# Optimization experiments

Hardware: AMD Instinct MI355X
Metric: run time of the kernel (lower is better)

Reference implementation:

```python
import jax, jax.numpy as jnp
import numpy as np

B, M, E, K = 8, 256, 128, 16
H, A, R, RMS = 1024, 256, 1024, 512
NEG = -1e25


def setup_inputs() -> dict:
    key = jax.random.key(0)
    ks = jax.random.split(key, 12)
    inp = {
        "mention_reprs": jax.random.normal(ks[0], (B, M, H), jnp.float32),
        "entities": jax.random.randint(ks[1], (B, E, K), 0, M),
        "entity_masks": jax.random.randint(ks[2], (B, E, K), 0, 2, dtype=jnp.int32),
        "relation_memory": jax.random.normal(ks[3], (R, RMS), jnp.float32),
        # GatedMILAttention params
        "Wv": jax.random.normal(ks[4], (A, H), jnp.float32) / np.sqrt(H),
        "bv": jnp.zeros((A,), jnp.float32),
        "Wu": jax.random.normal(ks[5], (A, H), jnp.float32) / np.sqrt(H),
        "bu": jnp.zeros((A,), jnp.float32),
        "Wa": jax.random.normal(ks[6], (1, A), jnp.float32) / np.sqrt(A),
        "ba": jnp.zeros((1,), jnp.float32),
        # relation memory read linear: Linear(RMS, H)
        "Wr": jax.random.normal(ks[7], (H, RMS), jnp.float32) / np.sqrt(RMS),
        "br": jnp.zeros((H,), jnp.float32),
        # output linear: Linear(H + RMS, H)
        "Wo": jax.random.normal(ks[8], (H, H + RMS), jnp.float32) / np.sqrt(H + RMS),
        "bo": jnp.zeros((H,), jnp.float32),
    }
    return inp


def reference(mention_reprs, entities, entity_masks, relation_memory,
              Wv, bv, Wu, bu, Wa, ba, Wr, br, Wo, bo):
    # gather mention clusters: [B, E, K, H]
    clusters = jax.vmap(lambda m, e: m[e])(mention_reprs, entities)
    # gated MIL attention
    aV = jnp.tanh(jnp.einsum('bekh,ah->beka', clusters, Wv) + bv)
    aU = jax.nn.sigmoid(jnp.einsum('bekh,ah->beka', clusters, Wu) + bu)
    logits = jnp.einsum('beka,oa->beko', aV * aU, Wa) + ba  # [B,E,K,1]
    mask = entity_masks[..., None].astype(bool)
    logits = jnp.where(mask, logits, NEG)
    a = jax.nn.softmax(logits, axis=2)
    # weighted pooling over mentions: [B, E, H]
    entity_reprs = jnp.sum(a * clusters, axis=2)
    # relation memory read (memory detached for the read projection)
    s_w = jax.lax.stop_gradient(relation_memory) @ Wr.T + br        # [R, H]
    s = jnp.einsum('beh,rh->ber', entity_reprs, s_w)                # [B, E, R]
    s = jnp.einsum('ber,rm->bem', s, relation_memory)               # [B, E, RMS]
    out = jnp.concatenate([entity_reprs, s], axis=-1) @ Wo.T + bo   # [B, E, H]
    return out  # dropout is identity at inference
```

## Files before the change

### kernel.cpp

```cpp
#include <hip/hip_runtime.h>
#include <cstdint>
#include <cstddef>

#define NEG_ (-1e25f)

typedef __bf16 bf16x8 __attribute__((ext_vector_type(8)));
typedef float  f32x4  __attribute__((ext_vector_type(4)));
typedef short  s16x8  __attribute__((ext_vector_type(8)));
typedef const __attribute__((address_space(1))) void* gas_t;
typedef __attribute__((address_space(3))) void* las_t;

#define MFMA16 __builtin_amdgcn_mfma_f32_16x16x32_bf16

__device__ __forceinline__ short f2bf(float f) {
  union { float f; unsigned u; } v; v.f = f;
  unsigned r = v.u + 0x7fffu + ((v.u >> 16) & 1u);
  return (short)(r >> 16);
}

__device__ __forceinline__ float bf2f(short s) {
  union { unsigned u; float f; } t; t.u = ((unsigned)(unsigned short)s) << 16;
  return t.f;
}

__device__ __forceinline__ s16x8 cvt8(const float* s) {
  bf16x8 r;
  #pragma unroll
  for (int j = 0; j < 8; ++j) r[j] = (__bf16)s[j];
  union { bf16x8 b; s16x8 s; } u; u.b = r; return u.s;
}

__device__ __forceinline__ void gload(const short* g, short* l) {
  __builtin_amdgcn_global_load_lds((gas_t)g, (las_t)l, 16, 0, 0);
}

struct Params {
  const float* ment; const int* ents; const int* msk;
  const float* rm; const float* Wv; const float* bv; const float* Wu;
  const float* bu; const float* Wa; const float* Wr; const float* br;
  const float* Wo; const float* bo; float* out;
  short *Xb, *Wvb, *Wub, *rmb, *Wrb, *Wo2b, *Wo1b, *swTb, *Ub, *Weffb, *erb;
  float *wpart, *cf, *gw2;
};

__global__ __launch_bounds__(256) void k0(Params p) {
  const int g = blockIdx.x * 256 + threadIdx.x;
  #pragma unroll
  for (int it = 0; it < 4; ++it) {
    int u = g + it * 131072;
    long e = (long)u * 8;
    const float* src; short* dst;
    if (u < 262144)      { src = p.ment + e;                     dst = p.Xb + e; }
    else if (u < 294912) { long o = e - 2097152; src = p.Wv + o; dst = p.Wvb + o; }
    else if (u < 327680) { long o = e - 2359296; src = p.Wu + o; dst = p.Wub + o; }
    else if (u < 393216) { long o = e - 2621440; src = p.rm + o; dst = p.rmb + o; }
    else if (u < 458752) { long o = e - 3145728; src = p.Wr + o; dst = p.Wrb + o; }
    else                 { long o = e - 3670016;
                           src = p.Wo + (o >> 9) * 1536 + 1024 + (o & 511);
                           dst = p.Wo2b + o; }
    float t[8];
    *(float4*)t       = *(const float4*)src;
    *(float4*)(t + 4) = *(const float4*)(src + 4);
    *(s16x8*)dst = cvt8(t);
  }
}

template <int NT, int EPI>
__device__ void g64(const short* __restrict__ A, int lda,
                    const short* __restrict__ B, int ldb,
                    void* __restrict__ C, int ldc, int m0, int n0,
                    const short* __restrict__ w1, const float* __restrict__ e0,
                    const float* __restrict__ e1, const float* __restrict__ e2,
                    short* lds) {
  short* As = lds;
  short* Bs = lds + 16384;
  const int tid = threadIdx.x, wave = tid >> 6, lane = tid & 63;
  const int quad = lane >> 4, l16 = lane & 15;
  const int wm = (wave & 1) * 32, wn = (wave >> 1) * 32;
  const int srow = tid >> 2, scol = (tid & 3) * 8;
  const short* Ag = A + (long)(m0 + srow) * lda + scol;
  const short* Bg = B + (long)(n0 + srow) * ldb + scol;
  const int wb = wave * 512;
  auto issue = [&](int kt) {
    int buf = kt & 7; int ko = kt * 32;
    gload(Ag + ko, As + buf * 2048 + wb);
    gload(Bg + ko, Bs + buf * 2048 + wb);
  };
  f32x4 acc[2][2] = {};
  issue(0); issue(1); issue(2); issue(3); issue(4); issue(5);
  for (int kt = 0; kt < NT; ++kt) {
    int rem = NT - 1 - kt;
    if (rem >= 5)      asm volatile("s_waitcnt vmcnt(10)" ::: "memory");
    else if (rem == 4) asm volatile("s_waitcnt vmcnt(8)" ::: "memory");
    else if (rem == 3) asm volatile("s_waitcnt vmcnt(6)" ::: "memory");
    else if (rem == 2) asm volatile("s_waitcnt vmcnt(4)" ::: "memory");
    else if (rem == 1) asm volatile("s_waitcnt vmcnt(2)" ::: "memory");
    else               asm volatile("s_waitcnt vmcnt(0)" ::: "memory");
    asm volatile("s_barrier" ::: "memory");
    if (kt + 6 < NT) issue(kt + 6);
    const short* as = As + (kt & 7) * 2048;
    const short* bs = Bs + (kt & 7) * 2048;
    bf16x8 a0 = *(const bf16x8*)&as[(wm + l16) * 32 + quad * 8];
    bf16x8 a1 = *(const bf16x8*)&as[(wm + 16 + l16) * 32 + quad * 8];
    bf16x8 b0 = *(const bf16x8*)&bs[(wn + l16) * 32 + quad * 8];
    bf16x8 b1 = *(const bf16x8*)&bs[(wn + 16 + l16) * 32 + quad * 8];
    acc[0][0] = MFMA16(a0, b0, acc[0][0], 0, 0, 0);
    acc[0][1] = MFMA16(a0, b1, acc[0][1], 0, 0, 0);
    acc[1][0] = MFMA16(a1, b0, acc[1][0], 0, 0, 0);
    acc[1][1] = MFMA16(a1, b1, acc[1][1], 0, 0, 0);
  }
  #pragma unroll
  for (int i = 0; i < 2; ++i)
    #pragma unroll
    for (int j = 0; j < 2; ++j) {
      int col = n0 + wn + j * 16 + l16;
      #pragma unroll
      for (int r = 0; r < 4; ++r) {
        int row = m0 + wm + i * 16 + quad * 4 + r;
        float v = acc[i][j][r];
        if constexpr (EPI == 0) {
          ((short*)C)[(long)row * ldc + col] = f2bf(v);
        } else if constexpr (EPI == 1) {
          v += bf2f(w1[(long)row * 1024 + col]);
          ((short*)C)[(long)row * ldc + col] = f2bf(v);
        } else {
          v += e0[col] + e1[row] * e2[col];
          ((float*)C)[(long)row * ldc + col] = v;
        }
      }
    }
}

__device__ void vu_ring(int mi, int ni, const Params& p, short* lds, float* red) {
  short* As  = lds;
  short* Bvs = lds + 6 * 1024;
  short* Bus = lds + 6 * 1024 + 6 * 2048;
  const int tid = threadIdx.x, wave = tid >> 6, lane = tid & 63;
  const int quad = lane >> 4, l16 = lane & 15;
  const int wm = (wave & 1) * 16, wn = (wave >> 1) * 32;
  const int m0 = mi * 32, n0 = ni * 64;
  const int srow = tid >> 2, scol = (tid & 3) * 8;
  const short* Ag  = p.Xb  + (long)(m0 + srow) * 1024 + scol;
  const short* Bvg = p.Wvb + (long)(n0 + srow) * 1024 + scol;
  const short* Bug = p.Wub + (long)(n0 + srow) * 1024 + scol;
  const int wb = wave * 512;
  auto issue = [&](int kt) {
    int buf = kt % 6; int ko = kt * 32;
    if (wave < 2)
      gload(Ag + ko, As + buf * 1024 + wb);
    gload(Bvg + ko, Bvs + buf * 2048 + wb);
    gload(Bug + ko, Bus + buf * 2048 + wb);
  };
  f32x4 accv[2] = {}, accu[2] = {};
  issue(0); issue(1); issue(2); issue(3);
  for (int kt = 0; kt < 32; ++kt) {
    int rem = 31 - kt;
    if (wave < 2) {
      if (rem >= 3)      asm volatile("s_waitcnt vmcnt(9)" ::: "memory");
      else if (rem == 2) asm volatile("s_waitcnt vmcnt(6)" ::: "memory");
      else if (rem == 1) asm volatile("s_waitcnt vmcnt(3)" ::: "memory");
      else               asm volatile("s_waitcnt vmcnt(0)" ::: "memory");
    } else {
      if (rem >= 3)      asm volatile("s_waitcnt vmcnt(6)" ::: "memory");
      else if (rem == 2) asm volatile("s_waitcnt vmcnt(4)" ::: "memory");
      else if (rem == 1) asm volatile("s_waitcnt vmcnt(2)" ::: "memory");
      else               asm volatile("s_waitcnt vmcnt(0)" ::: "memory");
    }
    asm volatile("s_barrier" ::: "memory");
    if (kt + 4 < 32) issue(kt + 4);
    const short* as  = As  + (kt % 6) * 1024;
    const short* bvs = Bvs + (kt % 6) * 2048;
    const short* bus = Bus + (kt % 6) * 2048;
    bf16x8 af = *(const bf16x8*)&as[(wm + l16) * 32 + quad * 8];
    bf16x8 v0 = *(const bf16x8*)&bvs[(wn + l16) * 32 + quad * 8];
    bf16x8 v1 = *(const bf16x8*)&bvs[(wn + 16 + l16) * 32 + quad * 8];
    bf16x8 u0 = *(const bf16x8*)&bus[(wn + l16) * 32 + quad * 8];
    bf16x8 u1 = *(const bf16x8*)&bus[(wn + 16 + l16) * 32 + quad * 8];
    accv[0] = MFMA16(af, v0, accv[0], 0, 0, 0);
    accv[1] = MFMA16(af, v1, accv[1], 0, 0, 0);
    accu[0] = MFMA16(af, u0, accu[0], 0, 0, 0);
    accu[1] = MFMA16(af, u1, accu[1], 0, 0, 0);
  }
  float wsum[4] = {0.f, 0.f, 0.f, 0.f};
  #pragma unroll
  for (int j = 0; j < 2; ++j) {
    int col = n0 + wn + j * 16 + l16;
    float bvc = p.bv[col], buc = p.bu[col], wac = p.Wa[col];
    #pragma unroll
    for (int r = 0; r < 4; ++r) {
      float vv = tanhf(accv[j][r] + bvc);
      float uu = accu[j][r] + buc;
      wsum[r] += (vv / (1.0f + expf(-uu))) * wac;
    }
  }
  #pragma unroll
  for (int r = 0; r < 4; ++r) {
    float s = wsum[r];
    s += __shfl_down(s, 8, 16);
    s += __shfl_down(s, 4, 16);
    s += __shfl_down(s, 2, 16);
    s += __shfl_down(s, 1, 16);
    if (l16 == 0) red[(wave >> 1) * 32 + wm + quad * 4 + r] = s;
  }
  __syncthreads();
  if (tid < 32) p.wpart[ni * 2048 + m0 + tid] = red[tid] + red[32 + tid];
}

__device__ void gw2_wave(int row, const Params& p) {
  const int lane = threadIdx.x & 63;
  const short* u = p.Ub + (long)row * 1024 + lane * 16;
  union { s16x8 s; bf16x8 b; } w0, w1;
  w0.s = *(const s16x8*)u;
  w1.s = *(const s16x8*)(u + 8);
  float s = 0.f;
  #pragma unroll
  for (int j = 0; j < 8; ++j) s += (float)w0.b[j] + (float)w1.b[j];
  #pragma unroll
  for (int off = 32; off > 0; off >>= 1) s += __shfl_down(s, off);
  if (lane == 0) p.gw2[row] = s;
}

__device__ void entity_wave(int be, const Params& p) {
  const int lane = threadIdx.x & 63;
  const int b = be >> 7;
  float a = NEG_; int idx = 0;
  if (lane < 16) {
    idx = p.ents[be * 16 + lane];
    int j = (b << 8) + idx;
    float lw = p.wpart[j] + p.wpart[2048 + j] + p.wpart[4096 + j] + p.wpart[6144 + j];
    a = p.msk[be * 16 + lane] ? lw : NEG_;
  }
  float m = a;
  m = fmaxf(m, __shfl_xor(m, 1, 16));
  m = fmaxf(m, __shfl_xor(m, 2, 16));
  m = fmaxf(m, __shfl_xor(m, 4, 16));
  m = fmaxf(m, __shfl_xor(m, 8, 16));
  float e = expf(a - m);
  float s = e;
  s += __shfl_xor(s, 1, 16);
  s += __shfl_xor(s, 2, 16);
  s += __shfl_xor(s, 4, 16);
  s += __shfl_xor(s, 8, 16);
  float aw = e / s;
  float ak[16]; int ik[16];
  #pragma unroll
  for (int k = 0; k < 16; ++k) { ak[k] = __shfl(aw, k); ik[k] = __shfl(idx, k); }
  const short* Xr = p.Xb + ((long)b << 18);
  const int h0 = lane * 16;
  float acc[16];
  #pragma unroll
  for (int t = 0; t < 16; ++t) acc[t] = 0.f;
  #pragma unroll
  for (int c = 0; c < 2; ++c) {
    s16x8 xv[8][2];
    #pragma unroll
    for (int k = 0; k < 8; ++k) {
      const short* xr = Xr + (long)ik[c * 8 + k] * 1024 + h0;
      xv[k][0] = *(const s16x8*)xr;
      xv[k][1] = *(const s16x8*)(xr + 8);
    }
    #pragma unroll
    for (int k = 0; k < 8; ++k) {
      union { s16x8 s; bf16x8 b; } u0, u1;
      u0.s = xv[k][0]; u1.s = xv[k][1];
      float akk = ak[c * 8 + k];
      #pragma unroll
      for (int t = 0; t < 8; ++t) {
        acc[t]     += akk * (float)u0.b[t];
        acc[8 + t] += akk * (float)u1.b[t];
      }
    }
  }
  short* er = p.erb + (long)be * 1024 + h0;
  *(s16x8*)er       = cvt8(acc);
  *(s16x8*)(er + 8) = cvt8(acc + 8);
  float c = 0.f;
  const float* brp = p.br + h0;
  #pragma unroll
  for (int t = 0; t < 16; ++t) c += acc[t] * brp[t];
  #pragma unroll
  for (int off = 32; off > 0; off >>= 1) c += __shfl_down(c, off);
  if (lane == 0) p.cf[be] = c;
}

__global__ __launch_bounds__(256) void k1(Params p) {
  __shared__ short lds[32768];
  __shared__ float red[64];
  const int blk = blockIdx.x;
  if (blk < 256) {
    vu_ring(blk & 63, blk >> 6, p, lds, red);
  } else if (blk < 512) {
    int q = blk - 256;
    g64<16, 0>(p.Wrb, 512, p.rmb, 512, p.swTb, 1024,
               (q >> 4) * 64, (q & 15) * 64, nullptr, nullptr, nullptr, nullptr, lds);
  } else if (blk < 768) {
    int q = blk - 512;
    g64<16, 0>(p.Wo2b, 512, p.rmb, 512, p.Ub, 1024,
               (q >> 4) * 64, (q & 15) * 64, nullptr, nullptr, nullptr, nullptr, lds);
  } else {
    int g = (blk - 768) * 256 + threadIdx.x;
    #pragma unroll
    for (int it = 0; it < 8; ++it) {
      long o = ((long)(g + it * 16384)) * 8;
      const float* src = p.Wo + (o >> 10) * 1536 + (o & 1023);
      float t[8];
      *(float4*)t       = *(const float4*)src;
      *(float4*)(t + 4) = *(const float4*)(src + 4);
      *(s16x8*)(p.Wo1b + o) = cvt8(t);
    }
  }
}

__global__ __launch_bounds__(256) void k2(Params p) {
  __shared__ short lds[32768];
  const int blk = blockIdx.x;
  if (blk < 256) {
    g64<32, 1>(p.Ub, 1024, p.swTb, 1024, p.Weffb, 1024,
               (blk >> 4) * 64, (blk & 15) * 64, p.Wo1b, nullptr, nullptr, nullptr, lds);
  } else {
    int q = blk - 256;
    int wave = threadIdx.x >> 6;
    gw2_wave(q * 4 + wave, p);
    entity_wave(q * 4 + wave, p);
  }
}

__global__ __launch_bounds__(256) void k3(Params p) {
  __shared__ short lds[32768];
  const int blk = blockIdx.x;
  g64<32, 2>(p.erb, 1024, p.Weffb, 1024, p.out, 1024,
             (blk >> 4) * 64, (blk & 15) * 64, nullptr, p.bo, p.cf, p.gw2, lds);
}

extern "C" void kernel_launch(void* const* d_in, const int* in_sizes, int n_in,
                              void* d_out, int out_size, void* d_ws, size_t ws_size,
                              hipStream_t stream) {
  (void)in_sizes; (void)n_in; (void)out_size; (void)ws_size;
  Params p;
  p.ment = (const float*)d_in[0];
  p.ents = (const int*)d_in[1];
  p.msk  = (const int*)d_in[2];
  p.rm   = (const float*)d_in[3];
  p.Wv   = (const float*)d_in[4];
  p.bv   = (const float*)d_in[5];
  p.Wu   = (const float*)d_in[6];
  p.bu   = (const float*)d_in[7];
  p.Wa   = (const float*)d_in[8];
  p.Wr   = (const float*)d_in[10];
  p.br   = (const float*)d_in[11];
  p.Wo   = (const float*)d_in[12];
  p.bo   = (const float*)d_in[13];
  p.out  = (float*)d_out;

  char* w = (char*)d_ws;
  auto alloc = [&](size_t bytes) {
    void* q = (void*)w; w += (bytes + 255) & ~(size_t)255; return q;
  };
  p.Xb    = (short*)alloc((size_t)2048 * 1024 * 2);
  p.Wvb   = (short*)alloc((size_t)256 * 1024 * 2);
  p.Wub   = (short*)alloc((size_t)256 * 1024 * 2);
  p.rmb   = (short*)alloc((size_t)1024 * 512 * 2);
  p.Wrb   = (short*)alloc((size_t)1024 * 512 * 2);
  p.Wo2b  = (short*)alloc((size_t)1024 * 512 * 2);
  p.Wo1b  = (short*)alloc((size_t)1024 * 1024 * 2);
  p.swTb  = (short*)alloc((size_t)1024 * 1024 * 2);
  p.Ub    = (short*)alloc((size_t)1024 * 1024 * 2);
  p.Weffb = (short*)alloc((size_t)1024 * 1024 * 2);
  p.erb   = (short*)alloc((size_t)1024 * 1024 * 2);
  p.wpart = (float*)alloc((size_t)4 * 2048 * 4);
  p.cf    = (float*)alloc((size_t)1024 * 4);
  p.gw2   = (float*)alloc((size_t)1024 * 4);

  k0<<<512, 256, 0, stream>>>(p);
  k1<<<832, 256, 0, stream>>>(p);
  k2<<<512, 256, 0, stream>>>(p);
  k3<<<256, 256, 0, stream>>>(p);
}
```

Baseline: 130.8 us.

## Use 64x32 tiles for K2/K3 GEMMs, read Wo fp32 in epilogue, shrink LDS rings

Adds a 64x32-tile GEMM variant for the Weff and output GEMMs, doubling their block counts to 512 so more CUs are filled. The Weff epilogue now adds the fp32 Wo left half directly instead of a bf16 copy, so k1 no longer converts Wo1 and the Wo1b buffer is gone. Pipeline rings are cut from 8 to 6 stages (g64) and from 6 to 5 (vu_ring), with shallower prefetch, which lowers LDS per block and should allow more resident blocks. The trade-off is less latency hiding per block, lower MFMA reuse per tile, and uncoalesced strided fp32 reads of Wo in the epilogue.

```diff
diff --git a/kernel.cpp b/kernel.cpp
--- a/kernel.cpp
+++ b/kernel.cpp
@@ -18,11 +18,6 @@
   return (short)(r >> 16);
 }
 
-__device__ __forceinline__ float bf2f(short s) {
-  union { unsigned u; float f; } t; t.u = ((unsigned)(unsigned short)s) << 16;
-  return t.f;
-}
-
 __device__ __forceinline__ s16x8 cvt8(const float* s) {
   bf16x8 r;
   #pragma unroll
@@ -39,7 +34,7 @@
   const float* rm; const float* Wv; const float* bv; const float* Wu;
   const float* bu; const float* Wa; const float* Wr; const float* br;
   const float* Wo; const float* bo; float* out;
-  short *Xb, *Wvb, *Wub, *rmb, *Wrb, *Wo2b, *Wo1b, *swTb, *Ub, *Weffb, *erb;
+  short *Xb, *Wvb, *Wub, *rmb, *Wrb, *Wo2b, *swTb, *Ub, *Weffb, *erb;
   float *wpart, *cf, *gw2;
 };
 
@@ -65,15 +60,12 @@
   }
 }
 
-template <int NT, int EPI>
 __device__ void g64(const short* __restrict__ A, int lda,
                     const short* __restrict__ B, int ldb,
-                    void* __restrict__ C, int ldc, int m0, int n0,
-                    const short* __restrict__ w1, const float* __restrict__ e0,
-                    const float* __restrict__ e1, const float* __restrict__ e2,
+                    short* __restrict__ C, int ldc, int NT, int m0, int n0,
                     short* lds) {
   short* As = lds;
-  short* Bs = lds + 16384;
+  short* Bs = lds + 12288;
   const int tid = threadIdx.x, wave = tid >> 6, lane = tid & 63;
   const int quad = lane >> 4, l16 = lane & 15;
   const int wm = (wave & 1) * 32, wn = (wave >> 1) * 32;
@@ -82,24 +74,22 @@
   const short* Bg = B + (long)(n0 + srow) * ldb + scol;
   const int wb = wave * 512;
   auto issue = [&](int kt) {
-    int buf = kt & 7; int ko = kt * 32;
+    int buf = kt % 6; int ko = kt * 32;
     gload(Ag + ko, As + buf * 2048 + wb);
     gload(Bg + ko, Bs + buf * 2048 + wb);
   };
   f32x4 acc[2][2] = {};
-  issue(0); issue(1); issue(2); issue(3); issue(4); issue(5);
+  issue(0); issue(1); issue(2); issue(3);
   for (int kt = 0; kt < NT; ++kt) {
     int rem = NT - 1 - kt;
-    if (rem >= 5)      asm volatile("s_waitcnt vmcnt(10)" ::: "memory");
-    else if (rem == 4) asm volatile("s_waitcnt vmcnt(8)" ::: "memory");
-    else if (rem == 3) asm volatile("s_waitcnt vmcnt(6)" ::: "memory");
+    if (rem >= 3)      asm volatile("s_waitcnt vmcnt(6)" ::: "memory");
     else if (rem == 2) asm volatile("s_waitcnt vmcnt(4)" ::: "memory");
     else if (rem == 1) asm volatile("s_waitcnt vmcnt(2)" ::: "memory");
     else               asm volatile("s_waitcnt vmcnt(0)" ::: "memory");
     asm volatile("s_barrier" ::: "memory");
-    if (kt + 6 < NT) issue(kt + 6);
-    const short* as = As + (kt & 7) * 2048;
-    const short* bs = Bs + (kt & 7) * 2048;
+    if (kt + 4 < NT) issue(kt + 4);
+    const short* as = As + (kt % 6) * 2048;
+    const short* bs = Bs + (kt % 6) * 2048;
     bf16x8 a0 = *(const bf16x8*)&as[(wm + l16) * 32 + quad * 8];
     bf16x8 a1 = *(const bf16x8*)&as[(wm + 16 + l16) * 32 + quad * 8];
     bf16x8 b0 = *(const bf16x8*)&bs[(wn + l16) * 32 + quad * 8];
@@ -117,24 +107,78 @@
       #pragma unroll
       for (int r = 0; r < 4; ++r) {
         int row = m0 + wm + i * 16 + quad * 4 + r;
-        float v = acc[i][j][r];
-        if constexpr (EPI == 0) {
-          ((short*)C)[(long)row * ldc + col] = f2bf(v);
-        } else if constexpr (EPI == 1) {
-          v += bf2f(w1[(long)row * 1024 + col]);
-          ((short*)C)[(long)row * ldc + col] = f2bf(v);
-        } else {
-          v += e0[col] + e1[row] * e2[col];
-          ((float*)C)[(long)row * ldc + col] = v;
-        }
+        C[(long)row * ldc + col] = f2bf(acc[i][j][r]);
       }
     }
+}
+
+template <int NT, int EPI>
+__device__ void g6432(const short* __restrict__ A, int lda,
+                      const short* __restrict__ B, int ldb,
+                      void* __restrict__ C, int ldc, int m0, int n0,
+                      const float* __restrict__ e0, const float* __restrict__ e1,
+                      const float* __restrict__ e2, short* lds) {
+  short* As = lds;
+  short* Bs = lds + 12288;
+  const int tid = threadIdx.x, wave = tid >> 6, lane = tid & 63;
+  const int quad = lane >> 4, l16 = lane & 15;
+  const int wm = (wave & 1) * 32, wn = (wave >> 1) * 16;
+  const int srow = tid >> 2, scol = (tid & 3) * 8;
+  const short* Ag = A + (long)(m0 + srow) * lda + scol;
+  const short* Bg = B + (long)(n0 + srow) * ldb + scol;
+  const int wb = wave * 512;
+  auto issue = [&](int kt) {
+    int buf = kt % 6; int ko = kt * 32;
+    gload(Ag + ko, As + buf * 2048 + wb);
+    if (tid < 128) gload(Bg + ko, Bs + buf * 1024 + wb);
+  };
+  f32x4 acc[2] = {};
+  issue(0); issue(1); issue(2); issue(3);
+  for (int kt = 0; kt < NT; ++kt) {
+    int rem = NT - 1 - kt;
+    if (wave < 2) {
+      if (rem >= 3)      asm volatile("s_waitcnt vmcnt(6)" ::: "memory");
+      else if (rem == 2) asm volatile("s_waitcnt vmcnt(4)" ::: "memory");
+      else if (rem == 1) asm volatile("s_waitcnt vmcnt(2)" ::: "memory");
+      else               asm volatile("s_waitcnt vmcnt(0)" ::: "memory");
+    } else {
+      if (rem >= 3)      asm volatile("s_waitcnt vmcnt(3)" ::: "memory");
+      else if (rem == 2) asm volatile("s_waitcnt vmcnt(2)" ::: "memory");
+      else if (rem == 1) asm volatile("s_waitcnt vmcnt(1)" ::: "memory");
+      else               asm volatile("s_waitcnt vmcnt(0)" ::: "memory");
+    }
+    asm volatile("s_barrier" ::: "memory");
+    if (kt + 4 < NT) issue(kt + 4);
+    const short* as = As + (kt % 6) * 2048;
+    const short* bs = Bs + (kt % 6) * 1024;
+    bf16x8 a0 = *(const bf16x8*)&as[(wm + l16) * 32 + quad * 8];
+    bf16x8 a1 = *(const bf16x8*)&as[(wm + 16 + l16) * 32 + quad * 8];
+    bf16x8 b0 = *(const bf16x8*)&bs[(wn + l16) * 32 + quad * 8];
+    acc[0] = MFMA16(a0, b0, acc[0], 0, 0, 0);
+    acc[1] = MFMA16(a1, b0, acc[1], 0, 0, 0);
+  }
+  #pragma unroll
+  for (int i = 0; i < 2; ++i) {
+    int col = n0 + wn + l16;
+    #pragma unroll
+    for (int r = 0; r < 4; ++r) {
+      int row = m0 + wm + i * 16 + quad * 4 + r;
+      float v = acc[i][r];
+      if constexpr (EPI == 1) {
+        v += e0[(long)row * 1536 + col];
+        ((short*)C)[(long)row * ldc + col] = f2bf(v);
+      } else {
+        v += e0[col] + e1[row] * e2[col];
+        ((float*)C)[(long)row * ldc + col] = v;
+      }
+    }
+  }
 }
 
 __device__ void vu_ring(int mi, int ni, const Params& p, short* lds, float* red) {
   short* As  = lds;
-  short* Bvs = lds + 6 * 1024;
-  short* Bus = lds + 6 * 1024 + 6 * 2048;
+  short* Bvs = lds + 5 * 1024;
+  short* Bus = lds + 5 * 1024 + 5 * 2048;
   const int tid = threadIdx.x, wave = tid >> 6, lane = tid & 63;
   const int quad = lane >> 4, l16 = lane & 15;
   const int wm = (wave & 1) * 16, wn = (wave >> 1) * 32;
@@ -145,7 +189,7 @@
   const short* Bug = p.Wub + (long)(n0 + srow) * 1024 + scol;
   const int wb = wave * 512;
   auto issue = [&](int kt) {
-    int buf = kt % 6; int ko = kt * 32;
+    int buf = kt % 5; int ko = kt * 32;
     if (wave < 2)
       gload(Ag + ko, As + buf * 1024 + wb);
     gload(Bvg + ko, Bvs + buf * 2048 + wb);
@@ -168,9 +212,9 @@
     }
     asm volatile("s_barrier" ::: "memory");
     if (kt + 4 < 32) issue(kt + 4);
-    const short* as  = As  + (kt % 6) * 1024;
-    const short* bvs = Bvs + (kt % 6) * 2048;
-    const short* bus = Bus + (kt % 6) * 2048;
+    const short* as  = As  + (kt % 5) * 1024;
+    const short* bvs = Bvs + (kt % 5) * 2048;
+    const short* bus = Bus + (kt % 5) * 2048;
     bf16x8 af = *(const bf16x8*)&as[(wm + l16) * 32 + quad * 8];
     bf16x8 v0 = *(const bf16x8*)&bvs[(wn + l16) * 32 + quad * 8];
     bf16x8 v1 = *(const bf16x8*)&bvs[(wn + 16 + l16) * 32 + quad * 8];
@@ -284,41 +328,30 @@
 }
 
 __global__ __launch_bounds__(256) void k1(Params p) {
-  __shared__ short lds[32768];
+  __shared__ short lds[25600];
   __shared__ float red[64];
   const int blk = blockIdx.x;
   if (blk < 256) {
     vu_ring(blk & 63, blk >> 6, p, lds, red);
   } else if (blk < 512) {
     int q = blk - 256;
-    g64<16, 0>(p.Wrb, 512, p.rmb, 512, p.swTb, 1024,
-               (q >> 4) * 64, (q & 15) * 64, nullptr, nullptr, nullptr, nullptr, lds);
-  } else if (blk < 768) {
+    g64(p.Wrb, 512, p.rmb, 512, p.swTb, 1024, 16,
+        (q >> 4) * 64, (q & 15) * 64, lds);
+  } else {
     int q = blk - 512;
-    g64<16, 0>(p.Wo2b, 512, p.rmb, 512, p.Ub, 1024,
-               (q >> 4) * 64, (q & 15) * 64, nullptr, nullptr, nullptr, nullptr, lds);
+    g64(p.Wo2b, 512, p.rmb, 512, p.Ub, 1024, 16,
+        (q >> 4) * 64, (q & 15) * 64, lds);
+  }
+}
+
+__global__ __launch_bounds__(256) void k2(Params p) {
+  __shared__ short lds[18432];
+  const int blk = blockIdx.x;
+  if (blk < 512) {
+    g6432<32, 1>(p.Ub, 1024, p.swTb, 1024, p.Weffb, 1024,
+                 (blk >> 5) * 64, (blk & 31) * 32, p.Wo, nullptr, nullptr, lds);
   } else {
-    int g = (blk - 768) * 256 + threadIdx.x;
-    #pragma unroll
-    for (int it = 0; it < 8; ++it) {
-      long o = ((long)(g + it * 16384)) * 8;
-      const float* src = p.Wo + (o >> 10) * 1536 + (o & 1023);
-      float t[8];
-      *(float4*)t       = *(const float4*)src;
-      *(float4*)(t + 4) = *(const float4*)(src + 4);
-      *(s16x8*)(p.Wo1b + o) = cvt8(t);
-    }
-  }
-}
-
-__global__ __launch_bounds__(256) void k2(Params p) {
-  __shared__ short lds[32768];
-  const int blk = blockIdx.x;
-  if (blk < 256) {
-    g64<32, 1>(p.Ub, 1024, p.swTb, 1024, p.Weffb, 1024,
-               (blk >> 4) * 64, (blk & 15) * 64, p.Wo1b, nullptr, nullptr, nullptr, lds);
-  } else {
-    int q = blk - 256;
+    int q = blk - 512;
     int wave = threadIdx.x >> 6;
     gw2_wave(q * 4 + wave, p);
     entity_wave(q * 4 + wave, p);
@@ -326,10 +359,10 @@
 }
 
 __global__ __launch_bounds__(256) void k3(Params p) {
-  __shared__ short lds[32768];
+  __shared__ short lds[18432];
   const int blk = blockIdx.x;
-  g64<32, 2>(p.erb, 1024, p.Weffb, 1024, p.out, 1024,
-             (blk >> 4) * 64, (blk & 15) * 64, nullptr, p.bo, p.cf, p.gw2, lds);
+  g6432<32, 2>(p.erb, 1024, p.Weffb, 1024, p.out, 1024,
+               (blk >> 5) * 64, (blk & 31) * 32, p.bo, p.cf, p.gw2, lds);
 }
 
 extern "C" void kernel_launch(void* const* d_in, const int* in_sizes, int n_in,
@@ -362,7 +395,6 @@
   p.rmb   = (short*)alloc((size_t)1024 * 512 * 2);
   p.Wrb   = (short*)alloc((size_t)1024 * 512 * 2);
   p.Wo2b  = (short*)alloc((size_t)1024 * 512 * 2);
-  p.Wo1b  = (short*)alloc((size_t)1024 * 1024 * 2);
   p.swTb  = (short*)alloc((size_t)1024 * 1024 * 2);
   p.Ub    = (short*)alloc((size_t)1024 * 1024 * 2);
   p.Weffb = (short*)alloc((size_t)1024 * 1024 * 2);
@@ -372,7 +404,7 @@
   p.gw2   = (float*)alloc((size_t)1024 * 4);
 
   k0<<<512, 256, 0, stream>>>(p);
-  k1<<<832, 256, 0, stream>>>(p);
-  k2<<<512, 256, 0, stream>>>(p);
-  k3<<<256, 256, 0, stream>>>(p);
-}
+  k1<<<768, 256, 0, stream>>>(p);
+  k2<<<768, 256, 0, stream>>>(p);
+  k3<<<512, 256, 0, stream>>>(p);
+}
```

After: 131.8 us. About the same (+0.8%).
